# Kernel optimization log

Hardware: AMD Instinct MI355X
Metric: run time of the kernel (lower is better)

The kernel has to match this reference:

```python
import jax, jax.numpy as jnp
import numpy as np

N_DIMS = 1024
N_HEADS = 16
HEAD_DIM = N_DIMS // N_HEADS


def setup_inputs() -> dict:
    key = jax.random.key(0)
    k_x, k_wa, k_wp = jax.random.split(key, 3)
    x = jax.random.normal(k_x, (4, 2048, N_DIMS), dtype=jnp.float32)
    # nn.Linear weights stored [out, in]; apply as x @ W.T
    scale_a = 1.0 / np.sqrt(N_DIMS)
    w_attn = jax.random.uniform(k_wa, (3 * N_DIMS, N_DIMS), jnp.float32, -scale_a, scale_a)
    w_proj = jax.random.uniform(k_wp, (N_DIMS, N_DIMS), jnp.float32, -scale_a, scale_a)
    return {"x": x, "w_attn": w_attn, "w_proj": w_proj}


def reference(x, w_attn, w_proj):
    B, S, D = x.shape
    qkv = x @ w_attn.T                                  # [B, S, 3D]
    q, k, v = jnp.split(qkv, 3, axis=-1)
    # [B, H, S, Dh]
    def heads(t):
        return t.reshape(B, S, N_HEADS, HEAD_DIM).transpose(0, 2, 1, 3)
    q, k, v = heads(q), heads(k), heads(v)
    scores = jnp.einsum('bhqd,bhkd->bhqk', q, k) * (1.0 / np.sqrt(HEAD_DIM))
    causal = jnp.tril(jnp.ones((S, S), dtype=bool))
    scores = jnp.where(causal[None, None], scores, -jnp.inf)
    attn = jax.nn.softmax(scores, axis=-1)              # dropout: eval mode (identity)
    y = jnp.einsum('bhqk,bhkd->bhqd', attn, v)
    y = y.transpose(0, 2, 1, 3).reshape(B, S, D)
    return y @ w_proj.T
```

## Files before the change

### kernel.cpp

```cpp
#include <hip/hip_runtime.h>

typedef unsigned short ushort_t;
typedef __attribute__((ext_vector_type(8))) short bf16x8;
typedef __attribute__((ext_vector_type(4))) float f32x4;


__device__ __forceinline__ ushort_t f2bf(float f) {
    union { float f; unsigned u; } c; c.f = f;
    unsigned u = c.u;
    unsigned r = (u + 0x7fffu + ((u >> 16) & 1u)) >> 16;
    return (ushort_t)r;
}

__device__ __forceinline__ unsigned pk_bf16(float a, float b) {
    unsigned r;
    asm("v_cvt_pk_bf16_f32 %0, %1, %2" : "=v"(r) : "v"(a), "v"(b));
    return r;
}

__device__ __forceinline__ void gld_lds16(const ushort_t* g, ushort_t* l) {
    __builtin_amdgcn_global_load_lds(
        (const __attribute__((address_space(1))) void*)g,
        (__attribute__((address_space(3))) void*)l, 16, 0, 0);
}


__global__ __launch_bounds__(256) void convert_all(
    const float* __restrict__ x, const float* __restrict__ wa, const float* __restrict__ wp,
    ushort_t* __restrict__ xb, ushort_t* __restrict__ wab, ushort_t* __restrict__ wpb)
{
    const int i = blockIdx.x * blockDim.x + threadIdx.x;
    const float* src; ushort_t* dst; int j;
    if (i < 2097152)      { src = x;  dst = xb;  j = i; }
    else if (i < 2883584) { src = wa; dst = wab; j = i - 2097152; }
    else                  { src = wp; dst = wpb; j = i - 2883584; }
    const float4 f = ((const float4*)src)[j];
    ushort4 o;
    o.x = f2bf(f.x); o.y = f2bf(f.y); o.z = f2bf(f.z); o.w = f2bf(f.w);
    ((ushort4*)dst)[j] = o;
}


__global__ __launch_bounds__(256) void gemm_qkv(
    const ushort_t* __restrict__ A, const ushort_t* __restrict__ W,
    ushort_t* __restrict__ qo, ushort_t* __restrict__ ko, ushort_t* __restrict__ vto)
{
    constexpr int K = 1024;
    const int m0 = blockIdx.x * 128;
    const int n0 = blockIdx.y * 128;
    __shared__ alignas(16) ushort_t smem[16384];
    ushort_t* sA = smem;
    ushort_t* sB = smem + 8192;
    const int tid = threadIdx.x;
    const int wave = tid >> 6, lane = tid & 63;
    const int quad = lane >> 4, l16 = lane & 15;
    const int l8 = lane & 7;
    const int wm = (wave >> 1) << 6, wn = (wave & 1) << 6;
    const int srow8 = lane >> 3;
    const int sg = ((l8 ^ srow8) << 3);

    f32x4 acc[4][4] = {};
    const ushort_t* aRow0 = A + (size_t)(m0 + wave * 32 + srow8) * K + sg;
    const ushort_t* bRow0 = W + (size_t)(n0 + wave * 32 + srow8) * K + sg;

    for (int k0 = 0; k0 < K; k0 += 64) {
#pragma unroll
        for (int c = 0; c < 4; ++c) {
            gld_lds16(aRow0 + (size_t)c * 8 * K + k0, sA + (wave * 4 + c) * 512);
            gld_lds16(bRow0 + (size_t)c * 8 * K + k0, sB + (wave * 4 + c) * 512);
        }
        __syncthreads();
#pragma unroll
        for (int ks = 0; ks < 2; ++ks) {
            bf16x8 af[4], bfr[4];
#pragma unroll
            for (int f = 0; f < 4; ++f) {
                const int rg = (((ks * 4 + quad) ^ l8) << 3);
                af[f]  = *(const bf16x8*)(sA + (wm + f * 16 + l16) * 64 + rg);
                bfr[f] = *(const bf16x8*)(sB + (wn + f * 16 + l16) * 64 + rg);
            }
#pragma unroll
            for (int mf = 0; mf < 4; ++mf)
#pragma unroll
                for (int nf = 0; nf < 4; ++nf)
                    acc[mf][nf] = __builtin_amdgcn_mfma_f32_16x16x32_bf16(af[mf], bfr[nf], acc[mf][nf], 0, 0, 0);
        }
        __syncthreads();
    }

    const int which = n0 >> 10;
    ushort_t* sT = smem + wave * 2048;
    const int b  = (m0 + wm) >> 11;
    const int sb = (m0 + wm) & 2047;
    const int h  = ((n0 + wn) & 1023) >> 6;
    const int bh = b * 16 + h;

    if (which < 2) {
        ushort_t* go = (which == 0) ? qo : ko;
        const float qs1 = (which == 0) ? 0.18033688011112042f : 1.0f;
#pragma unroll
        for (int mf = 0; mf < 4; ++mf) {
#pragma unroll
            for (int nf = 0; nf < 4; ++nf)
#pragma unroll
                for (int i = 0; i < 4; ++i) {
                    const int mll = quad * 4 + i;
                    sT[mll * 64 + ((nf * 16 + l16) ^ (4 * (mll & 7)))] = f2bf(acc[mf][nf][i] * qs1);
                }
            __builtin_amdgcn_s_waitcnt(0);
#pragma unroll
            for (int p = 0; p < 4; ++p) {
                const int mll = p * 4 + quad;
                const ushort4 val = *(const ushort4*)(sT + mll * 64 + ((l16 * 4) ^ (4 * (mll & 7))));
                const int s = sb + mf * 16 + mll;
                *(ushort4*)(go + ((size_t)bh * 2048 + s) * 64 + l16 * 4) = val;
            }
            __builtin_amdgcn_s_waitcnt(0);
        }
    } else {
#pragma unroll
        for (int nf = 0; nf < 4; ++nf) {
#pragma unroll
            for (int mf = 0; mf < 4; ++mf) {
                ushort4 w;
                w.x = f2bf(acc[mf][nf][0]);
                w.y = f2bf(acc[mf][nf][1]);
                w.z = f2bf(acc[mf][nf][2]);
                w.w = f2bf(acc[mf][nf][3]);
                *(ushort4*)(sT + l16 * 64 + ((mf * 16 + quad * 4) ^ (4 * (l16 & 7)))) = w;
            }
            __builtin_amdgcn_s_waitcnt(0);
#pragma unroll
            for (int p = 0; p < 4; ++p) {
                const int nll = p * 4 + quad;
                const ushort4 val = *(const ushort4*)(sT + nll * 64 + ((l16 * 4) ^ (4 * (nll & 7))));
                const int dh = nf * 16 + nll;
                *(ushort4*)(vto + ((size_t)bh * 64 + dh) * 2048 + sb + l16 * 4) = val;
            }
            __builtin_amdgcn_s_waitcnt(0);
        }
    }
}


__global__ __launch_bounds__(256) void attn(
    const ushort_t* __restrict__ qg_, const ushort_t* __restrict__ kg_,
    const ushort_t* __restrict__ vg_, ushort_t* __restrict__ y)
{
    const int bh = blockIdx.x;
    const int b = bh >> 4, h = bh & 15;
    const int tid = threadIdx.x, wave = tid >> 6, lane = tid & 63;
    const int quad = lane >> 4, l16 = lane & 15;
    const int l8 = lane & 7;

    __shared__ alignas(16) ushort_t sQ[4096];
    __shared__ alignas(16) ushort_t sK[4096];
    __shared__ alignas(16) ushort_t sV[4096];

    const ushort_t* kg = kg_ + (size_t)bh * 2048 * 64;
    const ushort_t* vg = vg_ + (size_t)bh * 64 * 2048;

    const int srow8 = lane >> 3;
    const int sg = ((l8 ^ srow8) << 3);

    const int qy = 31 - (int)blockIdx.y;
    const int q0 = qy * 64;

    {
        const ushort_t* qg = qg_ + ((size_t)bh * 2048 + q0 + wave * 16) * 64;
#pragma unroll
        for (int c = 0; c < 2; ++c)
            gld_lds16(qg + (size_t)(c * 8 + srow8) * 64 + sg, sQ + (wave * 2 + c) * 512);
    }
    __builtin_amdgcn_s_waitcnt(0);

    bf16x8 bq[2];
#pragma unroll
    for (int ks = 0; ks < 2; ++ks)
        bq[ks] = *(const bf16x8*)(sQ + (wave * 16 + l16) * 64 + (((ks * 4 + quad) ^ l8) << 3));

    f32x4 oacc[4] = {};
    f32x4 lpv = {0.f, 0.f, 0.f, 0.f};

    const int wrow = q0 + wave * 16 + l16;

    for (int t = 0; t <= qy; ++t) {
        const int k0 = t * 64;
        __syncthreads();
#pragma unroll
        for (int c = 0; c < 2; ++c) {
            const int chunk = wave * 2 + c;
            gld_lds16(kg + (size_t)(k0 + chunk * 8 + srow8) * 64 + sg, sK + chunk * 512);
            gld_lds16(vg + (size_t)(chunk * 8 + srow8) * 2048 + k0 + sg, sV + chunk * 512);
        }
        __syncthreads();

        f32x4 sacc[4] = {};
#pragma unroll
        for (int ks = 0; ks < 2; ++ks) {
            bf16x8 ak[4];
#pragma unroll
            for (int kf = 0; kf < 4; ++kf)
                ak[kf] = *(const bf16x8*)(sK + (kf * 16 + l16) * 64 + (((ks * 4 + quad) ^ l8) << 3));
#pragma unroll
            for (int kf = 0; kf < 4; ++kf)
                sacc[kf] = __builtin_amdgcn_mfma_f32_16x16x32_bf16(ak[kf], bq[ks], sacc[kf], 0, 0, 0);
        }

        const bool diag = (t == qy);
        unsigned Xp0[4], Xp1[4];
#pragma unroll
        for (int kf = 0; kf < 4; ++kf) {
            float pv[4];
#pragma unroll
            for (int i = 0; i < 4; ++i) {
                float sv = sacc[kf][i];
                if (diag) {
                    const int cg = k0 + kf * 16 + quad * 4 + i;
                    sv = (cg <= wrow) ? sv : -3.0e38f;
                }
                pv[i] = __builtin_amdgcn_exp2f(sv);
                lpv[i] += pv[i];
            }
            Xp0[kf] = pk_bf16(pv[0], pv[1]);
            Xp1[kf] = pk_bf16(pv[2], pv[3]);
        }

        bf16x8 pa[2];
#pragma unroll
        for (int ks = 0; ks < 2; ++ks) {
            unsigned a0 = Xp0[2 * ks], b0 = Xp0[2 * ks + 1];
            asm("v_permlane32_swap_b32 %0, %1" : "+v"(a0), "+v"(b0));
            asm("v_permlane16_swap_b32 %0, %1" : "+v"(a0), "+v"(b0));
            unsigned a1 = Xp1[2 * ks], b1 = Xp1[2 * ks + 1];
            asm("v_permlane32_swap_b32 %0, %1" : "+v"(a1), "+v"(b1));
            asm("v_permlane16_swap_b32 %0, %1" : "+v"(a1), "+v"(b1));
            union { unsigned u4[4]; bf16x8 v; } P;
            P.u4[0] = a0; P.u4[1] = a1; P.u4[2] = b0; P.u4[3] = b1;
            pa[ks] = P.v;
        }

#pragma unroll
        for (int ks = 0; ks < 2; ++ks) {
            const int rgrp = (((ks * 4 + quad) ^ l8) << 3);
            bf16x8 vb[4];
#pragma unroll
            for (int nf = 0; nf < 4; ++nf)
                vb[nf] = *(const bf16x8*)(sV + (nf * 16 + l16) * 64 + rgrp);
#pragma unroll
            for (int nf = 0; nf < 4; ++nf)
                oacc[nf] = __builtin_amdgcn_mfma_f32_16x16x32_bf16(pa[ks], vb[nf], oacc[nf], 0, 0, 0);
        }
    }

    float rs = (lpv[0] + lpv[1]) + (lpv[2] + lpv[3]);
    rs += __shfl_xor(rs, 16);
    rs += __shfl_xor(rs, 32);
#pragma unroll
    for (int i = 0; i < 4; ++i) {
        const float inv = 1.0f / __shfl(rs, quad * 4 + i);
        const int r = q0 + wave * 16 + quad * 4 + i;
#pragma unroll
        for (int nf = 0; nf < 4; ++nf)
            y[((size_t)b * 2048 + r) * 1024 + h * 64 + nf * 16 + l16] =
                f2bf(oacc[nf][i] * inv);
    }
}


__global__ __launch_bounds__(256) void gemm_proj(
    const ushort_t* __restrict__ A, const ushort_t* __restrict__ W, float* __restrict__ out)
{
    constexpr int K = 1024;
    const int m0 = blockIdx.x * 128;
    const int n0 = blockIdx.y * 128;
    __shared__ alignas(16) ushort_t smem[16384];
    ushort_t* sA = smem;
    ushort_t* sB = smem + 8192;
    const int tid = threadIdx.x;
    const int wave = tid >> 6, lane = tid & 63;
    const int quad = lane >> 4, l16 = lane & 15;
    const int l8 = lane & 7;
    const int wm = (wave >> 1) << 6, wn = (wave & 1) << 6;
    const int srow8 = lane >> 3;
    const int sg = ((l8 ^ srow8) << 3);

    f32x4 acc[4][4] = {};
    const ushort_t* aRow0 = A + (size_t)(m0 + wave * 32 + srow8) * K + sg;
    const ushort_t* bRow0 = W + (size_t)(n0 + wave * 32 + srow8) * K + sg;

    for (int k0 = 0; k0 < K; k0 += 64) {
#pragma unroll
        for (int c = 0; c < 4; ++c) {
            gld_lds16(aRow0 + (size_t)c * 8 * K + k0, sA + (wave * 4 + c) * 512);
            gld_lds16(bRow0 + (size_t)c * 8 * K + k0, sB + (wave * 4 + c) * 512);
        }
        __syncthreads();
#pragma unroll
        for (int ks = 0; ks < 2; ++ks) {
            bf16x8 af[4], bfr[4];
#pragma unroll
            for (int f = 0; f < 4; ++f) {
                const int rg = (((ks * 4 + quad) ^ l8) << 3);
                af[f]  = *(const bf16x8*)(sA + (wm + f * 16 + l16) * 64 + rg);
                bfr[f] = *(const bf16x8*)(sB + (wn + f * 16 + l16) * 64 + rg);
            }
#pragma unroll
            for (int mf = 0; mf < 4; ++mf)
#pragma unroll
                for (int nf = 0; nf < 4; ++nf)
                    acc[mf][nf] = __builtin_amdgcn_mfma_f32_16x16x32_bf16(af[mf], bfr[nf], acc[mf][nf], 0, 0, 0);
        }
        __syncthreads();
    }

#pragma unroll
    for (int mf = 0; mf < 4; ++mf)
#pragma unroll
        for (int nf = 0; nf < 4; ++nf)
#pragma unroll
            for (int i = 0; i < 4; ++i) {
                const int m = m0 + wm + mf * 16 + quad * 4 + i;
                const int n = n0 + wn + nf * 16 + l16;
                out[(size_t)m * 1024 + n] = acc[mf][nf][i];
            }
}


extern "C" void kernel_launch(void* const* d_in, const int* in_sizes, int n_in,
                              void* d_out, int out_size, void* d_ws, size_t ws_size,
                              hipStream_t stream) {
    const float* x  = (const float*)d_in[0];
    const float* wa = (const float*)d_in[1];
    const float* wp = (const float*)d_in[2];
    float* out = (float*)d_out;

    char* ws = (char*)d_ws;
    ushort_t* xb  = (ushort_t*)(ws);
    ushort_t* wab = (ushort_t*)(ws + 16777216);
    ushort_t* wpb = (ushort_t*)(ws + 16777216 + 6291456);
    ushort_t* q   = (ushort_t*)(ws + 25165824);
    ushort_t* k   = (ushort_t*)(ws + 41943040);
    ushort_t* vt  = (ushort_t*)(ws + 58720256);
    ushort_t* y   = xb;

    convert_all<<<12288, 256, 0, stream>>>(x, wa, wp, xb, wab, wpb);

    gemm_qkv<<<dim3(64, 24), 256, 0, stream>>>(xb, wab, q, k, vt);
    attn<<<dim3(64, 32), 256, 0, stream>>>(q, k, vt, y);
    gemm_proj<<<dim3(64, 8), 256, 0, stream>>>(y, wpb, out);
}
```

Measured before the change: 225.9 us.

## Load attention Q/K/V fragments directly from global memory, dropping LDS staging and barriers

The attention kernel no longer stages Q, K and V tiles in shared memory. Each lane now loads its MFMA operand fragments straight from global memory, so the per-tile __syncthreads pairs and the LDS buffers go away. Launch bounds also ask for 4 blocks per CU to raise occupancy. The cost is that all four waves in a block fetch the same K/V tile separately, so each block issues four times the global load traffic and depends on L1/L2 hits. Load latency can also no longer be overlapped through async LDS copies.

```diff
diff --git a/kernel.cpp b/kernel.cpp
--- a/kernel.cpp
+++ b/kernel.cpp
@@ -143,7 +143,7 @@
 }
 
 
-__global__ __launch_bounds__(256) void attn(
+__global__ __launch_bounds__(256, 4) void attn(
     const ushort_t* __restrict__ qg_, const ushort_t* __restrict__ kg_,
     const ushort_t* __restrict__ vg_, ushort_t* __restrict__ y)
 {
@@ -151,61 +151,38 @@
     const int b = bh >> 4, h = bh & 15;
     const int tid = threadIdx.x, wave = tid >> 6, lane = tid & 63;
     const int quad = lane >> 4, l16 = lane & 15;
-    const int l8 = lane & 7;
-
-    __shared__ alignas(16) ushort_t sQ[4096];
-    __shared__ alignas(16) ushort_t sK[4096];
-    __shared__ alignas(16) ushort_t sV[4096];
-
-    const ushort_t* kg = kg_ + (size_t)bh * 2048 * 64;
-    const ushort_t* vg = vg_ + (size_t)bh * 64 * 2048;
-
-    const int srow8 = lane >> 3;
-    const int sg = ((l8 ^ srow8) << 3);
 
     const int qy = 31 - (int)blockIdx.y;
     const int q0 = qy * 64;
-
-    {
-        const ushort_t* qg = qg_ + ((size_t)bh * 2048 + q0 + wave * 16) * 64;
-#pragma unroll
-        for (int c = 0; c < 2; ++c)
-            gld_lds16(qg + (size_t)(c * 8 + srow8) * 64 + sg, sQ + (wave * 2 + c) * 512);
-    }
-    __builtin_amdgcn_s_waitcnt(0);
+    const int wrow = q0 + wave * 16 + l16;
+
+    const ushort_t* kg = kg_ + (size_t)bh * 2048 * 64 + l16 * 64 + quad * 8;
+    const ushort_t* vg = vg_ + (size_t)bh * 64 * 2048 + (size_t)l16 * 2048 + quad * 8;
 
     bf16x8 bq[2];
 #pragma unroll
     for (int ks = 0; ks < 2; ++ks)
-        bq[ks] = *(const bf16x8*)(sQ + (wave * 16 + l16) * 64 + (((ks * 4 + quad) ^ l8) << 3));
+        bq[ks] = *(const bf16x8*)(qg_ + ((size_t)bh * 2048 + wrow) * 64 + ks * 32 + quad * 8);
 
     f32x4 oacc[4] = {};
     f32x4 lpv = {0.f, 0.f, 0.f, 0.f};
 
-    const int wrow = q0 + wave * 16 + l16;
-
     for (int t = 0; t <= qy; ++t) {
         const int k0 = t * 64;
-        __syncthreads();
-#pragma unroll
-        for (int c = 0; c < 2; ++c) {
-            const int chunk = wave * 2 + c;
-            gld_lds16(kg + (size_t)(k0 + chunk * 8 + srow8) * 64 + sg, sK + chunk * 512);
-            gld_lds16(vg + (size_t)(chunk * 8 + srow8) * 2048 + k0 + sg, sV + chunk * 512);
-        }
-        __syncthreads();
+
+        bf16x8 ak[2][4];
+#pragma unroll
+        for (int ks = 0; ks < 2; ++ks)
+#pragma unroll
+            for (int kf = 0; kf < 4; ++kf)
+                ak[ks][kf] = *(const bf16x8*)(kg + (size_t)(k0 + kf * 16) * 64 + ks * 32);
 
         f32x4 sacc[4] = {};
 #pragma unroll
-        for (int ks = 0; ks < 2; ++ks) {
-            bf16x8 ak[4];
+        for (int ks = 0; ks < 2; ++ks)
 #pragma unroll
             for (int kf = 0; kf < 4; ++kf)
-                ak[kf] = *(const bf16x8*)(sK + (kf * 16 + l16) * 64 + (((ks * 4 + quad) ^ l8) << 3));
-#pragma unroll
-            for (int kf = 0; kf < 4; ++kf)
-                sacc[kf] = __builtin_amdgcn_mfma_f32_16x16x32_bf16(ak[kf], bq[ks], sacc[kf], 0, 0, 0);
-        }
+                sacc[kf] = __builtin_amdgcn_mfma_f32_16x16x32_bf16(ak[ks][kf], bq[ks], sacc[kf], 0, 0, 0);
 
         const bool diag = (t == qy);
         unsigned Xp0[4], Xp1[4];
@@ -242,11 +219,10 @@
 
 #pragma unroll
         for (int ks = 0; ks < 2; ++ks) {
-            const int rgrp = (((ks * 4 + quad) ^ l8) << 3);
             bf16x8 vb[4];
 #pragma unroll
             for (int nf = 0; nf < 4; ++nf)
-                vb[nf] = *(const bf16x8*)(sV + (nf * 16 + l16) * 64 + rgrp);
+                vb[nf] = *(const bf16x8*)(vg + (size_t)nf * 16 * 2048 + k0 + ks * 32);
 #pragma unroll
             for (int nf = 0; nf < 4; ++nf)
                 oacc[nf] = __builtin_amdgcn_mfma_f32_16x16x32_bf16(pa[ks], vb[nf], oacc[nf], 0, 0, 0);
```

After: 413.7 us. 1.83x slower.
